# Optimization experiments

Measured on AMD Instinct MI355X. Metric: run time of the kernel, lower is better.

## Reference

```python
import jax, jax.numpy as jnp
import numpy as np

B, S, D = 4, 2048, 2048   # batch, seq, hidden
E, F, K = 8, 1024, 2      # experts, expert ffn dim, top-k
SF = 1024                 # shared-expert ffn dim
EPS = 1e-6


def setup_inputs() -> dict:
    key = jax.random.key(0)
    ks = jax.random.split(key, 9)
    g = lambda k, shape, scale: (jax.random.normal(k, shape, jnp.float32) * scale)
    return {
        "x": g(ks[0], (B, S, D), 1.0),
        "rms_weight": jnp.ones((D,), jnp.float32),
        "router_w": g(ks[1], (D, E), 0.02),
        "w_gate": g(ks[2], (E, D, F), 0.02),
        "w_up": g(ks[3], (E, D, F), 0.02),
        "w_down": g(ks[4], (E, F, D), 0.02),
        "sw_gate": g(ks[5], (D, SF), 0.02),
        "sw_up": g(ks[6], (D, SF), 0.02),
        "sw_down": g(ks[7], (SF, D), 0.02),
    }


def _rmsnorm(x, w, eps=EPS):
    var = jnp.mean(x * x, axis=-1, keepdims=True)
    return x * jax.lax.rsqrt(var + eps) * w


def reference(x, rms_weight, router_w, w_gate, w_up, w_down, sw_gate, sw_up, sw_down):
    b, s, d = x.shape
    e = router_w.shape[1]
    h = _rmsnorm(x, rms_weight)
    ht = h.reshape(-1, d)                      # [T, D] tokens
    t = ht.shape[0]

    # Router: softmax over experts, top-k, renormalize selected weights
    logits = ht @ router_w                     # [T, E]
    probs = jax.nn.softmax(logits, axis=-1)
    topv, topi = jax.lax.top_k(probs, K)       # [T, K]
    topv = topv / jnp.sum(topv, axis=-1, keepdims=True)
    # dense [T, E] combine weights (zero for non-selected experts)
    w_dense = jnp.zeros((t, e), ht.dtype).at[jnp.arange(t)[:, None], topi].set(topv)

    # Expert SwiGLU MLPs (grouped GEMM expressed densely over experts)
    g = jnp.einsum('td,edf->tef', ht, w_gate)  # [T, E, F]
    u = jnp.einsum('td,edf->tef', ht, w_up)
    eo = jnp.einsum('tef,efd->ted', jax.nn.silu(g) * u, w_down)  # [T, E, D]
    moe = jnp.einsum('te,ted->td', w_dense, eo)                   # weighted combine

    # Shared expert (SwiGLU)
    sh = (jax.nn.silu(ht @ sw_gate) * (ht @ sw_up)) @ sw_down

    return (moe + sh).reshape(b, s, d)
```

## Files before the change

kernel.cpp:

```cpp
#include <hip/hip_runtime.h>
#include <stdint.h>

#define T_TOK 8192
#define DDIM  2048
#define NEXP  8
#define FDIM  1024
#define CAP   25600
#define NT_M  200
#define BK    64
#define GXT   16
#define NBLK  (GXT * NT_M)
#define CPX   (NBLK / 8)

typedef __bf16 bf16x8 __attribute__((ext_vector_type(8)));
typedef float  f32x4  __attribute__((ext_vector_type(4)));

typedef const __attribute__((address_space(1))) uint32_t* as1_u32;
typedef __attribute__((address_space(3))) uint32_t* as3_u32;

__device__ __forceinline__ void gload16(const void* g, void* l) {
  __builtin_amdgcn_global_load_lds((as1_u32)g, (as3_u32)l, 16, 0, 0);
}
__device__ __forceinline__ float bf2f(uint16_t u) {
  union { uint32_t i; float f; } v; v.i = ((uint32_t)u) << 16; return v.f;
}
__device__ __forceinline__ uint16_t f2bf(float f) {
  union { float f; uint32_t i; } v; v.f = f;
  uint32_t i = v.i;
  i += 0x7FFFu + ((i >> 16) & 1u);
  return (uint16_t)(i >> 16);
}
__device__ __forceinline__ void mk_offs(const int* __restrict__ counts, int* o) {
  int a = 0;
  #pragma unroll
  for (int e = 0; e < NEXP; e++) { o[e] = a; a += (counts[e] + 127) & ~127; }
  o[8] = a; o[9] = a + T_TOK;
}

__global__ __launch_bounds__(256) void k_rms_router(
    const float* __restrict__ x, const float* __restrict__ rmsw,
    const float* __restrict__ router_w, uint16_t* __restrict__ h,
    int* __restrict__ topi, float* __restrict__ topw, int* __restrict__ counts)
{
  int wv = threadIdx.x >> 6, lane = threadIdx.x & 63;
  int t = blockIdx.x * 4 + wv;
  const float* xr = x + (size_t)t * DDIM;

  float4 xv[8], wv8[8];
  #pragma unroll
  for (int j = 0; j < 8; j++) {
    xv[j]  = ((const float4*)xr)[j * 64 + lane];
    wv8[j] = ((const float4*)rmsw)[j * 64 + lane];
  }
  float ss = 0.f;
  #pragma unroll
  for (int j = 0; j < 8; j++)
    ss += xv[j].x * xv[j].x + xv[j].y * xv[j].y + xv[j].z * xv[j].z + xv[j].w * xv[j].w;
  #pragma unroll
  for (int m = 32; m >= 1; m >>= 1) ss += __shfl_xor(ss, m, 64);
  float scale = rsqrtf(ss * (1.0f / DDIM) + 1e-6f);

  float hv[8][4];
  #pragma unroll
  for (int j = 0; j < 8; j++) {
    hv[j][0] = xv[j].x * scale * wv8[j].x;
    hv[j][1] = xv[j].y * scale * wv8[j].y;
    hv[j][2] = xv[j].z * scale * wv8[j].z;
    hv[j][3] = xv[j].w * scale * wv8[j].w;
    ushort4 hw;
    hw.x = f2bf(hv[j][0]); hw.y = f2bf(hv[j][1]);
    hw.z = f2bf(hv[j][2]); hw.w = f2bf(hv[j][3]);
    ((ushort4*)(h + (size_t)t * DDIM))[j * 64 + lane] = hw;
  }

  float lp[8] = {0, 0, 0, 0, 0, 0, 0, 0};
  #pragma unroll
  for (int j = 0; j < 8; j++) {
    #pragma unroll
    for (int c = 0; c < 4; c++) {
      int d = (j * 64 + lane) * 4 + c;
      const float* rw = router_w + (size_t)d * NEXP;
      float4 a = ((const float4*)rw)[0];
      float4 b = ((const float4*)rw)[1];
      float hj = hv[j][c];
      lp[0] += hj * a.x; lp[1] += hj * a.y; lp[2] += hj * a.z; lp[3] += hj * a.w;
      lp[4] += hj * b.x; lp[5] += hj * b.y; lp[6] += hj * b.z; lp[7] += hj * b.w;
    }
  }
  #pragma unroll
  for (int m = 32; m >= 1; m >>= 1) {
    #pragma unroll
    for (int e = 0; e < 8; e++) lp[e] += __shfl_xor(lp[e], m, 64);
  }
  if (lane == 0) {
    int i0 = 0;
    for (int e = 1; e < 8; e++) if (lp[e] > lp[i0]) i0 = e;
    int i1 = (i0 == 0) ? 1 : 0;
    for (int e = 0; e < 8; e++) if (e != i0 && lp[e] > lp[i1]) i1 = e;
    float p0 = 1.f / (1.f + expf(lp[i1] - lp[i0]));
    topi[t * 2] = i0; topi[t * 2 + 1] = i1;
    topw[t * 2] = p0; topw[t * 2 + 1] = 1.f - p0;
    atomicAdd(&counts[i0], 1);
    atomicAdd(&counts[i1], 1);
  }
}

__global__ __launch_bounds__(256) void k_scatter(
    const int* __restrict__ topi, const float* __restrict__ topw,
    const int* __restrict__ counts, int* __restrict__ cursor,
    int* __restrict__ tokslot, float* __restrict__ wtrow)
{
  int offs[10];
  mk_offs(counts, offs);
  int idx = blockIdx.x * 256 + threadIdx.x;
  if (idx < T_TOK * 2) {
    int t = idx >> 1, k = idx & 1;
    int e = topi[idx];
    int slot = atomicAdd(&cursor[e], 1);
    int row = offs[e] + slot;
    tokslot[row] = t * 4 + k;
    wtrow[row] = topw[idx];
  } else {
    int t = idx - T_TOK * 2;
    int row = offs[8] + t;
    tokslot[row] = t * 4 + 2;
    wtrow[row] = 1.0f;
  }
}

__global__ __launch_bounds__(256) void k_tr_all(
    const float* __restrict__ wg, const float* __restrict__ wu,
    const float* __restrict__ sg, const float* __restrict__ su,
    const float* __restrict__ wd, const float* __restrict__ sd,
    uint16_t* __restrict__ wgT, uint16_t* __restrict__ wuT,
    uint16_t* __restrict__ sgT, uint16_t* __restrict__ suT,
    uint16_t* __restrict__ wdT, uint16_t* __restrict__ sdT)
{
  __shared__ float tile[32][33];
  int flat = blockIdx.x;
  const float* src; uint16_t* dst;
  int R, C, r0, c0;
  if (flat < 36864) {
    int z = flat >> 11, rem = flat & 2047;
    R = DDIM; C = FDIM;
    r0 = (rem >> 5) << 5;
    c0 = (rem & 31) << 5;
    if (z < 8)       { src = wg + (size_t)z * DDIM * FDIM;       dst = wgT + (size_t)z * FDIM * DDIM; }
    else if (z < 16) { src = wu + (size_t)(z - 8) * DDIM * FDIM; dst = wuT + (size_t)(z - 8) * FDIM * DDIM; }
    else if (z == 16){ src = sg; dst = sgT; }
    else             { src = su; dst = suT; }
  } else {
    int f2 = flat - 36864;
    int z = f2 >> 11, rem = f2 & 2047;
    R = FDIM; C = DDIM;
    r0 = (rem >> 6) << 5;
    c0 = (rem & 63) << 5;
    if (z < 8) { src = wd + (size_t)z * FDIM * DDIM; dst = wdT + (size_t)z * DDIM * FDIM; }
    else       { src = sd; dst = sdT; }
  }
  int tx = threadIdx.x & 31, ty = threadIdx.x >> 5;
  #pragma unroll
  for (int i = 0; i < 4; i++)
    tile[ty + 8 * i][tx] = src[(size_t)(r0 + ty + 8 * i) * C + c0 + tx];
  __syncthreads();
  #pragma unroll
  for (int i = 0; i < 4; i++)
    dst[(size_t)(c0 + ty + 8 * i) * R + r0 + tx] = f2bf(tile[tx][ty + 8 * i]);
}

#define BUFA(c) (ldsu + (size_t)(c) * 16384)
#define BUFB(c) (ldsu + 8192 + (size_t)(c) * 16384)

#define XCD_REMAP()                                                            \
  int flat_ = blockIdx.y * GXT + blockIdx.x;                                   \
  int nf_ = (flat_ & 7) * CPX + (flat_ >> 3);                                  \
  int bx = nf_ & (GXT - 1);                                                    \
  int by = nf_ / GXT;

#define STAGE8(T, C) do {                                                     \
  _Pragma("unroll") for (int i_ = 0; i_ < 4; i_++) {                          \
    int G_ = w * 256 + i_ * 64 + lane;                                        \
    gload16(aSrc[i_] + (size_t)(T) * BK, BUFA(C) + G_ * 8);                   \
    gload16(bSrc[i_] + (size_t)(T) * BK, BUFB(C) + G_ * 8);                   \
  } } while (0)

#define COMPUTE_TILE(curA, curB) do {                                         \
  _Pragma("unroll") for (int ks_ = 0; ks_ < 2; ks_++) {                       \
    int ce_ = ks_ * 32 + ((lane >> 4) << 3);                                  \
    bf16x8 av_[4], bv_[4];                                                    \
    _Pragma("unroll") for (int m_ = 0; m_ < 4; m_++) {                        \
      int rr_ = wr * 64 + m_ * 16 + (lane & 15);                              \
      av_[m_] = *(const bf16x8*)((curA) + rr_ * 64 + (ce_ ^ ((rr_ & 7) << 3))); \
    }                                                                         \
    _Pragma("unroll") for (int n_ = 0; n_ < 4; n_++) {                        \
      int rr_ = wc * 64 + n_ * 16 + (lane & 15);                              \
      bv_[n_] = *(const bf16x8*)((curB) + rr_ * 64 + (ce_ ^ ((rr_ & 7) << 3))); \
    }                                                                         \
    __builtin_amdgcn_s_setprio(1);                                            \
    _Pragma("unroll") for (int m_ = 0; m_ < 4; m_++)                          \
    _Pragma("unroll") for (int n_ = 0; n_ < 4; n_++)                          \
      acc[m_][n_] = __builtin_amdgcn_mfma_f32_16x16x32_bf16(av_[m_], bv_[n_], acc[m_][n_], 0, 0, 0); \
    __builtin_amdgcn_s_setprio(0);                                            \
  } } while (0)

__global__ __launch_bounds__(256, 2) void k_stage1(
    const uint16_t* __restrict__ h, const uint16_t* __restrict__ wgT,
    const uint16_t* __restrict__ wuT, const uint16_t* __restrict__ sgT,
    const uint16_t* __restrict__ suT, const int* __restrict__ counts,
    const int* __restrict__ tokslot, uint16_t* __restrict__ A_int)
{
  __shared__ __align__(16) uint16_t ldsu[32768];

  int offs[10];
  mk_offs(counts, offs);
  XCD_REMAP();
  int row0 = by * 128;
  int end = offs[9];
  if (row0 >= end) return;
  int e = 0;
  #pragma unroll 1
  for (; e < 9; e++) if (row0 >= offs[e] && row0 < offs[e + 1]) break;
  const uint16_t* bg = (e < NEXP) ? wgT + (size_t)e * FDIM * DDIM : sgT;
  const uint16_t* bu = (e < NEXP) ? wuT + (size_t)e * FDIM * DDIM : suT;
  int f0 = bx * 64;

  int tid = threadIdx.x, lane = tid & 63, w = tid >> 6;
  int wr = w & 1, wc = w >> 1;

  const uint16_t* aSrc[4];
  const uint16_t* bSrc[4];
  #pragma unroll
  for (int i = 0; i < 4; i++) {
    int G = w * 256 + i * 64 + lane;
    int r = G >> 3, sl = G & 7;
    int gl = sl ^ (r & 7);
    int ts = tokslot[row0 + r];
    int tok = ts < 0 ? 0 : (ts >> 2);
    aSrc[i] = h + (size_t)tok * DDIM + gl * 8;
    int b = r >> 4;
    int fc = f0 + ((b >> 1) << 4) + (r & 15);
    const uint16_t* wbase = (b & 1) ? bu : bg;
    bSrc[i] = wbase + (size_t)fc * DDIM + gl * 8;
  }

  f32x4 acc[4][4] = {};
  const int NT = DDIM / BK;

  STAGE8(0, 0);
  __syncthreads();

  #pragma unroll 1
  for (int t = 0; t < NT; ++t) {
    int cur = t & 1;
    if (t + 1 < NT) STAGE8(t + 1, cur ^ 1);
    const uint16_t* curA = BUFA(cur);
    const uint16_t* curB = BUFB(cur);
    COMPUTE_TILE(curA, curB);
    __syncthreads();
  }

  #pragma unroll
  for (int m = 0; m < 4; m++) {
    #pragma unroll
    for (int p = 0; p < 2; p++) {
      #pragma unroll
      for (int r = 0; r < 4; r++) {
        int row = row0 + wr * 64 + m * 16 + ((lane >> 4) << 2) + r;
        int col = f0 + wc * 32 + p * 16 + (lane & 15);
        float g = acc[m][2 * p][r];
        float u = acc[m][2 * p + 1][r];
        float a = (g / (1.f + expf(-g))) * u;
        A_int[(size_t)row * FDIM + col] = f2bf(a);
      }
    }
  }
}

__global__ __launch_bounds__(256, 2) void k_stage2(
    const uint16_t* __restrict__ A_int, const uint16_t* __restrict__ wdT,
    const uint16_t* __restrict__ sdT, const int* __restrict__ counts,
    const int* __restrict__ tokslot, const float* __restrict__ wtrow,
    uint16_t* __restrict__ eo, float* __restrict__ out)
{
  __shared__ __align__(16) uint16_t ldsu[32768];

  int offs[10];
  mk_offs(counts, offs);
  XCD_REMAP();
  int row0 = by * 128;
  int end = offs[9];
  if (row0 >= end) return;
  int e = 0;
  #pragma unroll 1
  for (; e < 9; e++) if (row0 >= offs[e] && row0 < offs[e + 1]) break;
  const uint16_t* bw = (e < NEXP) ? wdT + (size_t)e * DDIM * FDIM : sdT;
  int d0 = bx * 128;

  int tid = threadIdx.x, lane = tid & 63, w = tid >> 6;
  int wr = w & 1, wc = w >> 1;

  const uint16_t* aSrc[4];
  const uint16_t* bSrc[4];
  #pragma unroll
  for (int i = 0; i < 4; i++) {
    int G = w * 256 + i * 64 + lane;
    int r = G >> 3, sl = G & 7;
    int gl = sl ^ (r & 7);
    aSrc[i] = A_int + (size_t)(row0 + r) * FDIM + gl * 8;
    bSrc[i] = bw + (size_t)(d0 + r) * FDIM + gl * 8;
  }

  f32x4 acc[4][4] = {};
  const int NT = FDIM / BK;

  STAGE8(0, 0);
  __syncthreads();

  #pragma unroll 1
  for (int t = 0; t < NT; ++t) {
    int cur = t & 1;
    if (t + 1 < NT) STAGE8(t + 1, cur ^ 1);
    const uint16_t* curA = BUFA(cur);
    const uint16_t* curB = BUFB(cur);
    COMPUTE_TILE(curA, curB);
    __syncthreads();
  }

  #pragma unroll
  for (int m = 0; m < 4; m++) {
    #pragma unroll
    for (int r = 0; r < 4; r++) {
      int grow = row0 + wr * 64 + m * 16 + ((lane >> 4) << 2) + r;
      int ts = tokslot[grow];
      if (ts < 0) continue;
      int tok = ts >> 2, slot = ts & 3;
      if (slot == 2) {
        size_t obase = (size_t)tok * DDIM;
        #pragma unroll
        for (int n = 0; n < 4; n++) {
          int col = d0 + wc * 64 + n * 16 + (lane & 15);
          out[obase + col] = acc[m][n][r];
        }
      } else {
        float wt = wtrow[grow];
        size_t obase = ((size_t)tok * 2 + slot) * DDIM;
        #pragma unroll
        for (int n = 0; n < 4; n++) {
          int col = d0 + wc * 64 + n * 16 + (lane & 15);
          eo[obase + col] = f2bf(acc[m][n][r] * wt);
        }
      }
    }
  }
}

__global__ __launch_bounds__(256) void k_final(
    const uint16_t* __restrict__ eo, float* __restrict__ out)
{
  int tok = blockIdx.x;
  int col = threadIdx.x * 8;
  const uint16_t* e0 = eo + ((size_t)tok * 2) * DDIM + col;
  const uint16_t* e1 = eo + ((size_t)tok * 2 + 1) * DDIM + col;
  float* op = out + (size_t)tok * DDIM + col;
  ushort4 a0 = *(const ushort4*)(e0);
  ushort4 a1 = *(const ushort4*)(e0 + 4);
  ushort4 b0 = *(const ushort4*)(e1);
  ushort4 b1 = *(const ushort4*)(e1 + 4);
  float4 s0 = *(const float4*)(op);
  float4 s1 = *(const float4*)(op + 4);
  float4 o0, o1;
  o0.x = s0.x + bf2f(a0.x) + bf2f(b0.x);
  o0.y = s0.y + bf2f(a0.y) + bf2f(b0.y);
  o0.z = s0.z + bf2f(a0.z) + bf2f(b0.z);
  o0.w = s0.w + bf2f(a0.w) + bf2f(b0.w);
  o1.x = s1.x + bf2f(a1.x) + bf2f(b1.x);
  o1.y = s1.y + bf2f(a1.y) + bf2f(b1.y);
  o1.z = s1.z + bf2f(a1.z) + bf2f(b1.z);
  o1.w = s1.w + bf2f(a1.w) + bf2f(b1.w);
  *(float4*)(op) = o0;
  *(float4*)(op + 4) = o1;
}

extern "C" void kernel_launch(void* const* d_in, const int* in_sizes, int n_in,
                              void* d_out, int out_size, void* d_ws, size_t ws_size,
                              hipStream_t stream) {
  (void)in_sizes; (void)n_in; (void)out_size;
  const float* x    = (const float*)d_in[0];
  const float* rmsw = (const float*)d_in[1];
  const float* rtw  = (const float*)d_in[2];
  const float* wg   = (const float*)d_in[3];
  const float* wu   = (const float*)d_in[4];
  const float* wd   = (const float*)d_in[5];
  const float* sg   = (const float*)d_in[6];
  const float* su   = (const float*)d_in[7];
  const float* sd   = (const float*)d_in[8];
  float* out = (float*)d_out;

  char* base = (char*)d_ws;
  size_t off_b = 0;
  auto place = [&](size_t bytes) { size_t r = off_b; off_b += (bytes + 255) & ~(size_t)255; return r; };
  size_t o_topi    = place((size_t)T_TOK * 2 * 4);
  size_t o_topw    = place((size_t)T_TOK * 2 * 4);
  size_t o_counts  = place(64);
  size_t o_cursor  = place(64);
  size_t o_tokslot = place((size_t)CAP * 4);
  size_t o_wtrow   = place((size_t)CAP * 4);
  size_t o_h   = place((size_t)T_TOK * DDIM * 2);
  size_t o_wgT = place((size_t)NEXP * FDIM * DDIM * 2);
  size_t o_wuT = place((size_t)NEXP * FDIM * DDIM * 2);
  size_t o_sgT = place((size_t)FDIM * DDIM * 2);
  size_t o_suT = place((size_t)FDIM * DDIM * 2);
  size_t o_wdT = place((size_t)NEXP * DDIM * FDIM * 2);
  size_t o_sdT = place((size_t)DDIM * FDIM * 2);
  size_t o_Ai  = place((size_t)CAP * FDIM * 2);
  size_t o_eo  = o_h;
  size_t NEED = off_b;
  if (ws_size < NEED) return;

  int*      topi    = (int*)(base + o_topi);
  float*    topw    = (float*)(base + o_topw);
  int*      counts  = (int*)(base + o_counts);
  int*      cursor  = (int*)(base + o_cursor);
  int*      tokslot = (int*)(base + o_tokslot);
  float*    wtrow   = (float*)(base + o_wtrow);
  uint16_t* h       = (uint16_t*)(base + o_h);
  uint16_t* wgT     = (uint16_t*)(base + o_wgT);
  uint16_t* wuT     = (uint16_t*)(base + o_wuT);
  uint16_t* sgT     = (uint16_t*)(base + o_sgT);
  uint16_t* suT     = (uint16_t*)(base + o_suT);
  uint16_t* wdT     = (uint16_t*)(base + o_wdT);
  uint16_t* sdT     = (uint16_t*)(base + o_sdT);
  uint16_t* Ai      = (uint16_t*)(base + o_Ai);
  uint16_t* eo      = (uint16_t*)(base + o_eo);

  hipMemsetAsync(counts, 0, 512, stream);
  hipMemsetAsync(tokslot, 0xFF, (size_t)CAP * 4, stream);

  k_tr_all<<<55296, 256, 0, stream>>>(wg, wu, sg, su, wd, sd,
                                      wgT, wuT, sgT, suT, wdT, sdT);

  k_rms_router<<<T_TOK / 4, 256, 0, stream>>>(x, rmsw, rtw, h, topi, topw, counts);
  k_scatter<<<(T_TOK * 3) / 256, 256, 0, stream>>>(topi, topw, counts, cursor, tokslot, wtrow);

  k_stage1<<<dim3(GXT, NT_M), 256, 0, stream>>>(h, wgT, wuT, sgT, suT, counts, tokslot, Ai);
  k_stage2<<<dim3(GXT, NT_M), 256, 0, stream>>>(Ai, wdT, sdT, counts, tokslot, wtrow, eo, out);
  k_final<<<T_TOK, 256, 0, stream>>>(eo, out);
}
```

Baseline: 740.9 us.

## Merge weight transpose and RMSNorm/router into one prep kernel, vectorize transpose

Combines the weight transpose/convert kernel and the RMSNorm+router kernel into a single launch, with block index selecting the role, so the two independent jobs run concurrently and one launch gap disappears. The transpose also switches from scalar 4-pass loads/stores to one float4 load and one ushort4 store per thread. Risks include LDS bank conflicts in the new strided tile reads and the router blocks being scheduled only after all transpose blocks.

```diff
diff --git a/kernel.cpp b/kernel.cpp
--- a/kernel.cpp
+++ b/kernel.cpp
@@ -11,6 +11,7 @@
 #define GXT   16
 #define NBLK  (GXT * NT_M)
 #define CPX   (NBLK / 8)
+#define NTR   55296
 
 typedef __bf16 bf16x8 __attribute__((ext_vector_type(8)));
 typedef float  f32x4  __attribute__((ext_vector_type(4)));
@@ -37,71 +38,117 @@
   o[8] = a; o[9] = a + T_TOK;
 }
 
-__global__ __launch_bounds__(256) void k_rms_router(
+__global__ __launch_bounds__(256) void k_prep(
+    const float* __restrict__ wg, const float* __restrict__ wu,
+    const float* __restrict__ sg, const float* __restrict__ su,
+    const float* __restrict__ wd, const float* __restrict__ sd,
     const float* __restrict__ x, const float* __restrict__ rmsw,
-    const float* __restrict__ router_w, uint16_t* __restrict__ h,
-    int* __restrict__ topi, float* __restrict__ topw, int* __restrict__ counts)
+    const float* __restrict__ router_w,
+    uint16_t* __restrict__ wgT, uint16_t* __restrict__ wuT,
+    uint16_t* __restrict__ sgT, uint16_t* __restrict__ suT,
+    uint16_t* __restrict__ wdT, uint16_t* __restrict__ sdT,
+    uint16_t* __restrict__ h, int* __restrict__ topi,
+    float* __restrict__ topw, int* __restrict__ counts)
 {
-  int wv = threadIdx.x >> 6, lane = threadIdx.x & 63;
-  int t = blockIdx.x * 4 + wv;
-  const float* xr = x + (size_t)t * DDIM;
-
-  float4 xv[8], wv8[8];
-  #pragma unroll
-  for (int j = 0; j < 8; j++) {
-    xv[j]  = ((const float4*)xr)[j * 64 + lane];
-    wv8[j] = ((const float4*)rmsw)[j * 64 + lane];
-  }
-  float ss = 0.f;
-  #pragma unroll
-  for (int j = 0; j < 8; j++)
-    ss += xv[j].x * xv[j].x + xv[j].y * xv[j].y + xv[j].z * xv[j].z + xv[j].w * xv[j].w;
-  #pragma unroll
-  for (int m = 32; m >= 1; m >>= 1) ss += __shfl_xor(ss, m, 64);
-  float scale = rsqrtf(ss * (1.0f / DDIM) + 1e-6f);
-
-  float hv[8][4];
-  #pragma unroll
-  for (int j = 0; j < 8; j++) {
-    hv[j][0] = xv[j].x * scale * wv8[j].x;
-    hv[j][1] = xv[j].y * scale * wv8[j].y;
-    hv[j][2] = xv[j].z * scale * wv8[j].z;
-    hv[j][3] = xv[j].w * scale * wv8[j].w;
-    ushort4 hw;
-    hw.x = f2bf(hv[j][0]); hw.y = f2bf(hv[j][1]);
-    hw.z = f2bf(hv[j][2]); hw.w = f2bf(hv[j][3]);
-    ((ushort4*)(h + (size_t)t * DDIM))[j * 64 + lane] = hw;
-  }
-
-  float lp[8] = {0, 0, 0, 0, 0, 0, 0, 0};
-  #pragma unroll
-  for (int j = 0; j < 8; j++) {
-    #pragma unroll
-    for (int c = 0; c < 4; c++) {
-      int d = (j * 64 + lane) * 4 + c;
-      const float* rw = router_w + (size_t)d * NEXP;
-      float4 a = ((const float4*)rw)[0];
-      float4 b = ((const float4*)rw)[1];
-      float hj = hv[j][c];
-      lp[0] += hj * a.x; lp[1] += hj * a.y; lp[2] += hj * a.z; lp[3] += hj * a.w;
-      lp[4] += hj * b.x; lp[5] += hj * b.y; lp[6] += hj * b.z; lp[7] += hj * b.w;
-    }
-  }
-  #pragma unroll
-  for (int m = 32; m >= 1; m >>= 1) {
-    #pragma unroll
-    for (int e = 0; e < 8; e++) lp[e] += __shfl_xor(lp[e], m, 64);
-  }
-  if (lane == 0) {
-    int i0 = 0;
-    for (int e = 1; e < 8; e++) if (lp[e] > lp[i0]) i0 = e;
-    int i1 = (i0 == 0) ? 1 : 0;
-    for (int e = 0; e < 8; e++) if (e != i0 && lp[e] > lp[i1]) i1 = e;
-    float p0 = 1.f / (1.f + expf(lp[i1] - lp[i0]));
-    topi[t * 2] = i0; topi[t * 2 + 1] = i1;
-    topw[t * 2] = p0; topw[t * 2 + 1] = 1.f - p0;
-    atomicAdd(&counts[i0], 1);
-    atomicAdd(&counts[i1], 1);
+  __shared__ float tile[32][33];
+  int flat = blockIdx.x;
+  if (flat < NTR) {
+    const float* src; uint16_t* dst;
+    int R, C, r0, c0;
+    if (flat < 36864) {
+      int z = flat >> 11, rem = flat & 2047;
+      R = DDIM; C = FDIM;
+      r0 = (rem >> 5) << 5;
+      c0 = (rem & 31) << 5;
+      if (z < 8)       { src = wg + (size_t)z * DDIM * FDIM;       dst = wgT + (size_t)z * FDIM * DDIM; }
+      else if (z < 16) { src = wu + (size_t)(z - 8) * DDIM * FDIM; dst = wuT + (size_t)(z - 8) * FDIM * DDIM; }
+      else if (z == 16){ src = sg; dst = sgT; }
+      else             { src = su; dst = suT; }
+    } else {
+      int f2 = flat - 36864;
+      int z = f2 >> 11, rem = f2 & 2047;
+      R = FDIM; C = DDIM;
+      r0 = (rem >> 6) << 5;
+      c0 = (rem & 63) << 5;
+      if (z < 8) { src = wd + (size_t)z * FDIM * DDIM; dst = wdT + (size_t)z * DDIM * FDIM; }
+      else       { src = sd; dst = sdT; }
+    }
+    int tx2 = threadIdx.x & 7;
+    int ty2 = threadIdx.x >> 3;
+    float4 v = *(const float4*)(src + (size_t)(r0 + ty2) * C + c0 + tx2 * 4);
+    tile[ty2][tx2 * 4 + 0] = v.x;
+    tile[ty2][tx2 * 4 + 1] = v.y;
+    tile[ty2][tx2 * 4 + 2] = v.z;
+    tile[ty2][tx2 * 4 + 3] = v.w;
+    __syncthreads();
+    ushort4 o;
+    o.x = f2bf(tile[tx2 * 4 + 0][ty2]);
+    o.y = f2bf(tile[tx2 * 4 + 1][ty2]);
+    o.z = f2bf(tile[tx2 * 4 + 2][ty2]);
+    o.w = f2bf(tile[tx2 * 4 + 3][ty2]);
+    *(ushort4*)(dst + (size_t)(c0 + ty2) * R + r0 + tx2 * 4) = o;
+  } else {
+    int wv = threadIdx.x >> 6, lane = threadIdx.x & 63;
+    int t = (flat - NTR) * 4 + wv;
+    const float* xr = x + (size_t)t * DDIM;
+
+    float4 xv[8], wv8[8];
+    #pragma unroll
+    for (int j = 0; j < 8; j++) {
+      xv[j]  = ((const float4*)xr)[j * 64 + lane];
+      wv8[j] = ((const float4*)rmsw)[j * 64 + lane];
+    }
+    float ss = 0.f;
+    #pragma unroll
+    for (int j = 0; j < 8; j++)
+      ss += xv[j].x * xv[j].x + xv[j].y * xv[j].y + xv[j].z * xv[j].z + xv[j].w * xv[j].w;
+    #pragma unroll
+    for (int m = 32; m >= 1; m >>= 1) ss += __shfl_xor(ss, m, 64);
+    float scale = rsqrtf(ss * (1.0f / DDIM) + 1e-6f);
+
+    float hv[8][4];
+    #pragma unroll
+    for (int j = 0; j < 8; j++) {
+      hv[j][0] = xv[j].x * scale * wv8[j].x;
+      hv[j][1] = xv[j].y * scale * wv8[j].y;
+      hv[j][2] = xv[j].z * scale * wv8[j].z;
+      hv[j][3] = xv[j].w * scale * wv8[j].w;
+      ushort4 hw;
+      hw.x = f2bf(hv[j][0]); hw.y = f2bf(hv[j][1]);
+      hw.z = f2bf(hv[j][2]); hw.w = f2bf(hv[j][3]);
+      ((ushort4*)(h + (size_t)t * DDIM))[j * 64 + lane] = hw;
+    }
+
+    float lp[8] = {0, 0, 0, 0, 0, 0, 0, 0};
+    #pragma unroll
+    for (int j = 0; j < 8; j++) {
+      #pragma unroll
+      for (int c = 0; c < 4; c++) {
+        int d = (j * 64 + lane) * 4 + c;
+        const float* rw = router_w + (size_t)d * NEXP;
+        float4 a = ((const float4*)rw)[0];
+        float4 b = ((const float4*)rw)[1];
+        float hj = hv[j][c];
+        lp[0] += hj * a.x; lp[1] += hj * a.y; lp[2] += hj * a.z; lp[3] += hj * a.w;
+        lp[4] += hj * b.x; lp[5] += hj * b.y; lp[6] += hj * b.z; lp[7] += hj * b.w;
+      }
+    }
+    #pragma unroll
+    for (int m = 32; m >= 1; m >>= 1) {
+      #pragma unroll
+      for (int e = 0; e < 8; e++) lp[e] += __shfl_xor(lp[e], m, 64);
+    }
+    if (lane == 0) {
+      int i0 = 0;
+      for (int e = 1; e < 8; e++) if (lp[e] > lp[i0]) i0 = e;
+      int i1 = (i0 == 0) ? 1 : 0;
+      for (int e = 0; e < 8; e++) if (e != i0 && lp[e] > lp[i1]) i1 = e;
+      float p0 = 1.f / (1.f + expf(lp[i1] - lp[i0]));
+      topi[t * 2] = i0; topi[t * 2 + 1] = i1;
+      topw[t * 2] = p0; topw[t * 2 + 1] = 1.f - p0;
+      atomicAdd(&counts[i0], 1);
+      atomicAdd(&counts[i1], 1);
+    }
   }
 }
 
@@ -126,46 +173,6 @@
     tokslot[row] = t * 4 + 2;
     wtrow[row] = 1.0f;
   }
-}
-
-__global__ __launch_bounds__(256) void k_tr_all(
-    const float* __restrict__ wg, const float* __restrict__ wu,
-    const float* __restrict__ sg, const float* __restrict__ su,
-    const float* __restrict__ wd, const float* __restrict__ sd,
-    uint16_t* __restrict__ wgT, uint16_t* __restrict__ wuT,
-    uint16_t* __restrict__ sgT, uint16_t* __restrict__ suT,
-    uint16_t* __restrict__ wdT, uint16_t* __restrict__ sdT)
-{
-  __shared__ float tile[32][33];
-  int flat = blockIdx.x;
-  const float* src; uint16_t* dst;
-  int R, C, r0, c0;
-  if (flat < 36864) {
-    int z = flat >> 11, rem = flat & 2047;
-    R = DDIM; C = FDIM;
-    r0 = (rem >> 5) << 5;
-    c0 = (rem & 31) << 5;
-    if (z < 8)       { src = wg + (size_t)z * DDIM * FDIM;       dst = wgT + (size_t)z * FDIM * DDIM; }
-    else if (z < 16) { src = wu + (size_t)(z - 8) * DDIM * FDIM; dst = wuT + (size_t)(z - 8) * FDIM * DDIM; }
-    else if (z == 16){ src = sg; dst = sgT; }
-    else             { src = su; dst = suT; }
-  } else {
-    int f2 = flat - 36864;
-    int z = f2 >> 11, rem = f2 & 2047;
-    R = FDIM; C = DDIM;
-    r0 = (rem >> 6) << 5;
-    c0 = (rem & 63) << 5;
-    if (z < 8) { src = wd + (size_t)z * FDIM * DDIM; dst = wdT + (size_t)z * DDIM * FDIM; }
-    else       { src = sd; dst = sdT; }
-  }
-  int tx = threadIdx.x & 31, ty = threadIdx.x >> 5;
-  #pragma unroll
-  for (int i = 0; i < 4; i++)
-    tile[ty + 8 * i][tx] = src[(size_t)(r0 + ty + 8 * i) * C + c0 + tx];
-  __syncthreads();
-  #pragma unroll
-  for (int i = 0; i < 4; i++)
-    dst[(size_t)(c0 + ty + 8 * i) * R + r0 + tx] = f2bf(tile[tx][ty + 8 * i]);
 }
 
 #define BUFA(c) (ldsu + (size_t)(c) * 16384)
@@ -436,10 +443,10 @@
   hipMemsetAsync(counts, 0, 512, stream);
   hipMemsetAsync(tokslot, 0xFF, (size_t)CAP * 4, stream);
 
-  k_tr_all<<<55296, 256, 0, stream>>>(wg, wu, sg, su, wd, sd,
-                                      wgT, wuT, sgT, suT, wdT, sdT);
-
-  k_rms_router<<<T_TOK / 4, 256, 0, stream>>>(x, rmsw, rtw, h, topi, topw, counts);
+  k_prep<<<NTR + T_TOK / 4, 256, 0, stream>>>(
+      wg, wu, sg, su, wd, sd, x, rmsw, rtw,
+      wgT, wuT, sgT, suT, wdT, sdT, h, topi, topw, counts);
+
   k_scatter<<<(T_TOK * 3) / 256, 256, 0, stream>>>(topi, topw, counts, cursor, tokslot, wtrow);
 
   k_stage1<<<dim3(GXT, NT_M), 256, 0, stream>>>(h, wgT, wuT, sgT, suT, counts, tokslot, Ai);
```

Result: no change. 730.5 us (-1.4%).
